# Kernel optimization log

Measured on AMD Instinct MI355X. Metric: run time of the kernel, lower is better.

## Reference

```python
import jax, jax.numpy as jnp
import numpy as np
import math

H = 8
D_MODEL = 4096
D_K = D_MODEL // H  # 512; Sk must equal D_K for the im_attn @ value matmul
B, SQ, SK = 4, 2048, 512


def _linear_params(key, fan_in, fan_out):
    kw, kb = jax.random.split(key)
    bound = 1.0 / math.sqrt(fan_in)
    W = jax.random.uniform(kw, (fan_out, fan_in), jnp.float32, -bound, bound)
    b = jax.random.uniform(kb, (fan_out,), jnp.float32, -bound, bound)
    return W, b


def setup_inputs() -> dict:
    key = jax.random.key(0)
    ks = jax.random.split(key, 8)
    query = jax.random.normal(ks[0], (B, SQ, D_MODEL), jnp.float32)
    k_in = jax.random.normal(ks[1], (B, SK, D_MODEL), jnp.float32)
    v_in = jax.random.normal(ks[2], (B, SK, D_MODEL), jnp.float32)
    image_feat = jax.random.normal(ks[3], (B, SK, D_MODEL), jnp.float32)
    W0, b0 = _linear_params(ks[4], D_MODEL, D_MODEL)
    W1, b1 = _linear_params(ks[5], D_MODEL, D_MODEL)
    W2, b2 = _linear_params(ks[6], D_MODEL, D_MODEL)
    W3, b3 = _linear_params(ks[7], D_MODEL, D_MODEL)  # reused for image_feat AND output proj (as in source)
    return {"query": query, "key": k_in, "value": v_in, "image_feat": image_feat,
            "W0": W0, "b0": b0, "W1": W1, "b1": b1, "W2": W2, "b2": b2, "W3": W3, "b3": b3}


def _split_heads(x):
    # [b, s, d_model] -> [b, h, s, d_k]
    b, s, _ = x.shape
    return x.reshape(b, s, H, D_K).transpose(0, 2, 1, 3)


def reference(query, key, value, image_feat, W0, b0, W1, b1, W2, b2, W3, b3):
    q = _split_heads(query @ W0.T + b0)        # [b,h,Sq,d_k]
    k = _split_heads(key @ W1.T + b1)          # [b,h,Sk,d_k]
    v = _split_heads(value @ W2.T + b2)        # [b,h,Sk,d_k]
    imf = _split_heads(image_feat @ W3.T + b3) # [b,h,Sk,d_k]

    scores = jnp.einsum('bhqd,bhkd->bhqk', q, k) / math.sqrt(D_K)  # [b,h,Sq,Sk]
    p_attn = jax.nn.softmax(scores, axis=-1)
    # second-stage attention over feature axis (Sk == d_k so shapes line up)
    im_attn = jax.nn.softmax(jnp.einsum('bhqk,bhkd->bhqd', p_attn, imf), axis=-1)  # [b,h,Sq,d_k]
    x = jnp.einsum('bhqs,bhsd->bhqd', im_attn, v)  # contracts d_k axis of im_attn with Sk axis of v

    x = x.transpose(0, 2, 1, 3).reshape(query.shape[0], -1, H * D_K)  # [b,Sq,d_model]
    return x @ W3.T + b3  # linears[-1] is the same (shared) 4th linear
```

## Files before the change

### kernel.cpp

```cpp
#include <hip/hip_runtime.h>
#include <hip/hip_bf16.h>
#include <stdint.h>

#define B_   4
#define H_   8
#define SQ_  2048
#define SK_  512
#define DM_  4096
#define DK_  512

typedef __bf16 bf16;
typedef __bf16 bf16x8 __attribute__((ext_vector_type(8)));
typedef float  fx4    __attribute__((ext_vector_type(4)));

typedef __attribute__((address_space(1))) void gv_t;
typedef __attribute__((address_space(3))) void lv_t;

__global__ void sniff_dtype(const uint32_t* __restrict__ q, int* __restrict__ flag)
{
    const int l = threadIdx.x;
    int cnt = 0;
    #pragma unroll
    for (int i = 0; i < 4; ++i) {
        const uint32_t u = q[l * 4 + i];
        const int e = (u >> 7) & 0xFF;
        cnt += (e >= 100 && e <= 135) ? 1 : 0;
    }
    #pragma unroll
    for (int s = 1; s < 64; s <<= 1) cnt += __shfl_xor(cnt, s);
    if (l == 0) *flag = (cnt < 150) ? 1 : 0;
}

__global__ __launch_bounds__(256) void cvt_to_bf16(
    const void* __restrict__ in, bf16* __restrict__ out, const int* __restrict__ flagp)
{
    const size_t i = ((size_t)blockIdx.x * 256 + threadIdx.x) * 8;
    if (*flagp) {
        const float4* p = (const float4*)((const float*)in + i);
        const float4 u0 = p[0], u1 = p[1];
        bf16x8 v;
        v[0] = (bf16)u0.x; v[1] = (bf16)u0.y; v[2] = (bf16)u0.z; v[3] = (bf16)u0.w;
        v[4] = (bf16)u1.x; v[5] = (bf16)u1.y; v[6] = (bf16)u1.z; v[7] = (bf16)u1.w;
        *(bf16x8*)(out + i) = v;
    } else {
        *(bf16x8*)(out + i) = *(const bf16x8*)((const bf16*)in + i);
    }
}

__global__ __launch_bounds__(256, 3) void gemm_bt(
    const bf16* __restrict__ A, const bf16* __restrict__ Bt,
    void* __restrict__ Cv, const void* __restrict__ biasv,
    int K, int lda, int ldb, int ldc, float alpha,
    long long sAb, long long sAh, long long sBb, long long sBh,
    long long sCb, long long sCh,
    const int* __restrict__ flagp, int ebits)
{
    __shared__ bf16 sA[128 * 64];
    __shared__ bf16 sB[128 * 64];

    const int fl = ebits ? *flagp : 0;
    const bool bias32 = fl && (ebits & 1);
    const bool c32    = fl && (ebits & 2);

    const int z = blockIdx.z;
    const int bz = z >> 3, hz = z & 7;
    const bf16* Ab = A  + (size_t)bz * sAb + (size_t)hz * sAh;
    const bf16* Bb = Bt + (size_t)bz * sBb + (size_t)hz * sBh;
    const size_t offC = (size_t)bz * sCb + (size_t)hz * sCh;

    const int n0 = blockIdx.x * 128;
    const int m0 = blockIdx.y * 128;

    const int t = threadIdx.x;
    const int w = t >> 6, l = t & 63;
    const int lrow = l >> 3, lcol = l & 7;
    const int wm = (w >> 1) * 64, wn = (w & 1) * 64;
    const int ml = l & 15, quad = l >> 4;

    const bf16* pa[4];
    const bf16* pb[4];
    #pragma unroll
    for (int i = 0; i < 4; ++i) {
        const int c = w * 4 + i;
        const int r = c * 8 + lrow;
        const int jj = lcol ^ (r & 7);
        pa[i] = Ab + (size_t)(m0 + r) * lda + jj * 8;
        pb[i] = Bb + (size_t)(n0 + r) * ldb + jj * 8;
    }

    fx4 acc[4][4];
    const fx4 zero = {0.f, 0.f, 0.f, 0.f};
    #pragma unroll
    for (int i = 0; i < 4; ++i)
        #pragma unroll
        for (int j = 0; j < 4; ++j) acc[i][j] = zero;

    for (int kt = 0; kt < K; kt += 64) {
        #pragma unroll
        for (int i = 0; i < 4; ++i) {
            const int c = w * 4 + i;
            __builtin_amdgcn_global_load_lds((gv_t*)(pa[i] + kt), (lv_t*)(sA + c * 512), 16, 0, 0);
            __builtin_amdgcn_global_load_lds((gv_t*)(pb[i] + kt), (lv_t*)(sB + c * 512), 16, 0, 0);
        }
        __syncthreads();

        #pragma unroll
        for (int kk = 0; kk < 64; kk += 32) {
            bf16x8 af[4], bfr[4];
            const int jbase = (kk >> 3) + quad;
            #pragma unroll
            for (int mi = 0; mi < 4; ++mi) {
                const int r = wm + mi * 16 + ml;
                af[mi] = *(const bf16x8*)&sA[r * 64 + ((jbase ^ (r & 7)) << 3)];
            }
            #pragma unroll
            for (int ni = 0; ni < 4; ++ni) {
                const int r = wn + ni * 16 + ml;
                bfr[ni] = *(const bf16x8*)&sB[r * 64 + ((jbase ^ (r & 7)) << 3)];
            }
            #pragma unroll
            for (int mi = 0; mi < 4; ++mi)
                #pragma unroll
                for (int ni = 0; ni < 4; ++ni)
                    acc[mi][ni] = __builtin_amdgcn_mfma_f32_16x16x32_bf16(
                        af[mi], bfr[ni], acc[mi][ni], 0, 0, 0);
        }
        __syncthreads();
    }

    #pragma unroll
    for (int ni = 0; ni < 4; ++ni) {
        const int cg = n0 + wn + ni * 16 + ml;
        const float bv = biasv ? (bias32 ? ((const float*)biasv)[cg] : (float)((const bf16*)biasv)[cg]) : 0.f;
        #pragma unroll
        for (int mi = 0; mi < 4; ++mi) {
            const int rg = m0 + wm + mi * 16 + quad * 4;
            #pragma unroll
            for (int r = 0; r < 4; ++r) {
                const float val = acc[mi][ni][r] * alpha + bv;
                const size_t idx = offC + (size_t)(rg + r) * ldc + cg;
                if (c32) ((float*)Cv)[idx] = val;
                else     ((bf16*)Cv)[idx] = (bf16)val;
            }
        }
    }
}

#define BARRIER   asm volatile("s_barrier" ::: "memory")
#define LGKM0     asm volatile("s_waitcnt lgkmcnt(0)" ::: "memory")
#define VM0       asm volatile("s_waitcnt vmcnt(0)" ::: "memory")
#define SCHED0    __builtin_amdgcn_sched_barrier(0)

#define LDS_FRAG(dst, base, fr, kI)                                               \
    dst = *(const bf16x8*)&base[(fr) * 64 + ((((kI) * 4 + quad) ^ ((fr) & 7)) << 3)]

#define READ_A(dst, sX, roff)                                                     \
    _Pragma("unroll")                                                             \
    for (int im_ = 0; im_ < 4; ++im_)                                             \
        _Pragma("unroll")                                                         \
        for (int kI_ = 0; kI_ < 2; ++kI_)                                         \
            LDS_FRAG(dst[im_][kI_], sX, R0 + (roff) + im_ * 16 + ml, kI_);

#define READ_B(dst, sX, coff)                                                     \
    _Pragma("unroll")                                                             \
    for (int in_ = 0; in_ < 2; ++in_)                                             \
        _Pragma("unroll")                                                         \
        for (int kI_ = 0; kI_ < 2; ++kI_)                                         \
            LDS_FRAG(dst[in_][kI_], sX, C0 + (coff) + in_ * 16 + ml, kI_);

#define MFMA_Q(mo, no, afr_, bfr_)                                                \
    __builtin_amdgcn_s_setprio(1);                                                \
    _Pragma("unroll")                                                             \
    for (int kI_ = 0; kI_ < 2; ++kI_)                                             \
        _Pragma("unroll")                                                         \
        for (int im_ = 0; im_ < 4; ++im_)                                         \
            _Pragma("unroll")                                                     \
            for (int in_ = 0; in_ < 2; ++in_)                                     \
                acc[(mo) + im_][(no) + in_] =                                     \
                    __builtin_amdgcn_mfma_f32_16x16x32_bf16(                      \
                        afr_[im_][kI_], bfr_[in_][kI_],                           \
                        acc[(mo) + im_][(no) + in_], 0, 0, 0);                    \
    __builtin_amdgcn_s_setprio(0);

#define STAGE_A(ts, sb)                                                           \
    do {                                                                          \
        _Pragma("unroll")                                                         \
        for (int h_ = 0; h_ < 2; ++h_)                                            \
            _Pragma("unroll")                                                     \
            for (int j_ = 0; j_ < 2; ++j_)                                        \
                __builtin_amdgcn_global_load_lds(                                 \
                    (gv_t*)(pA[h_][j_] + (size_t)(ts) * 64),                      \
                    (lv_t*)(&sm[sb][0][h_ * 8192 + (2 * w + j_) * 512]),          \
                    16, 0, 0);                                                    \
    } while (0)

#define STAGE_B(ts, sb, h)                                                        \
    do {                                                                          \
        _Pragma("unroll")                                                         \
        for (int j_ = 0; j_ < 2; ++j_)                                            \
            __builtin_amdgcn_global_load_lds(                                     \
                (gv_t*)(pB[h][j_] + (size_t)(ts) * 64),                           \
                (lv_t*)(&sm[sb][1][(h) * 8192 + (2 * w + j_) * 512]),             \
                16, 0, 0);                                                        \
    } while (0)

#define HALF_ITER(cb, ts, sb, dostage)                                            \
    do {                                                                          \
        const bf16* sA_ = &sm[cb][0][0];                                          \
        const bf16* sB_ = &sm[cb][1][0];                                          \
                                                                          \
        READ_A(afr, sA_, 0);                                                      \
        READ_B(b0r, sB_, 0);                                                      \
        if (dostage) { STAGE_A(ts, sb); }                                         \
        BARRIER; LGKM0; SCHED0;                                                   \
        MFMA_Q(0, 0, afr, b0r);                                                   \
        BARRIER;                                                                  \
                                                                          \
        READ_B(b1r, sB_, 32);                                                     \
        if (dostage) { STAGE_B(ts, sb, 0); }                                      \
        BARRIER; LGKM0; SCHED0;                                                   \
        MFMA_Q(0, 2, afr, b1r);                                                   \
        BARRIER;                                                                  \
                                                                          \
        READ_A(afr, sA_, 64);                                                     \
        if (dostage) { STAGE_B(ts, sb, 1); }                                      \
        BARRIER; LGKM0; SCHED0;                                                   \
        MFMA_Q(4, 2, afr, b1r);                                                   \
        BARRIER;                                                                  \
                             \
        MFMA_Q(4, 0, afr, b0r);                                                   \
        VM0;                                                                      \
        BARRIER;                                                                  \
    } while (0)

__global__ __launch_bounds__(512, 2) void gemm256(
    const bf16* __restrict__ A, const bf16* __restrict__ Bt,
    void* __restrict__ Cv, const void* __restrict__ biasv,
    int K, int lda, int ldb, int ldc, float alpha,
    long long sAb, long long sAh, long long sBb, long long sBh,
    long long sCb, long long sCh,
    const int* __restrict__ flagp, int ebits)
{
    __shared__ bf16 sm[2][2][256 * 64];

    const int fl = ebits ? *flagp : 0;
    const bool bias32 = fl && (ebits & 1);
    const bool c32    = fl && (ebits & 2);

    const int gX = gridDim.x, gY = gridDim.y;
    int idx = (blockIdx.z * gY + blockIdx.y) * gX + blockIdx.x;
    const int nwg = gX * gY * gridDim.z;
    if ((nwg & 7) == 0) idx = (idx & 7) * (nwg >> 3) + (idx >> 3);
    const int bx = idx % gX;
    const int tmpi = idx / gX;
    const int by = tmpi % gY;
    const int z  = tmpi / gY;

    const int bz = z >> 3, hz = z & 7;
    const bf16* Ab = A  + (size_t)bz * sAb + (size_t)hz * sAh;
    const bf16* Bb = Bt + (size_t)bz * sBb + (size_t)hz * sBh;
    const size_t offC = (size_t)bz * sCb + (size_t)hz * sCh;

    const int n0 = bx * 256;
    const int m0 = by * 256;

    const int t  = threadIdx.x;
    const int w  = t >> 6, l = t & 63;
    const int lrow = l >> 3, lcol = l & 7;
    const int wr = w >> 2, wc = w & 3;
    const int R0 = wr * 128, C0 = wc * 64;
    const int ml = l & 15, quad = l >> 4;

    const bf16* pA[2][2];
    const bf16* pB[2][2];
    #pragma unroll
    for (int h = 0; h < 2; ++h)
        #pragma unroll
        for (int j = 0; j < 2; ++j) {
            const int r = h * 128 + (2 * w + j) * 8 + lrow;
            const int jj = lcol ^ (r & 7);
            pA[h][j] = Ab + (size_t)(m0 + r) * lda + jj * 8;
            pB[h][j] = Bb + (size_t)(n0 + r) * ldb + jj * 8;
        }

    fx4 acc[8][4];
    const fx4 zero = {0.f, 0.f, 0.f, 0.f};
    #pragma unroll
    for (int i = 0; i < 8; ++i)
        #pragma unroll
        for (int j = 0; j < 4; ++j) acc[i][j] = zero;

    bf16x8 afr[4][2], b0r[2][2], b1r[2][2];

    const int nt  = K >> 6;
    const int nit = nt >> 1;

    STAGE_A(0, 0);
    STAGE_B(0, 0, 0);
    STAGE_B(0, 0, 1);
    VM0;
    BARRIER;

    for (int it = 0; it < nit; ++it) {
        HALF_ITER(0, 2 * it + 1, 1, true);
        HALF_ITER(1, 2 * it + 2, 0, (it + 1 < nit));
    }

    #pragma unroll
    for (int ni = 0; ni < 4; ++ni) {
        const int cg = n0 + C0 + ni * 16 + ml;
        const float bv = biasv ? (bias32 ? ((const float*)biasv)[cg] : (float)((const bf16*)biasv)[cg]) : 0.f;
        #pragma unroll
        for (int mi = 0; mi < 8; ++mi) {
            const int rg = m0 + R0 + mi * 16 + quad * 4;
            #pragma unroll
            for (int r = 0; r < 4; ++r) {
                const float val = acc[mi][ni][r] * alpha + bv;
                const size_t idx = offC + (size_t)(rg + r) * ldc + cg;
                if (c32) ((float*)Cv)[idx] = val;
                else     ((bf16*)Cv)[idx] = (bf16)val;
            }
        }
    }
}

__global__ __launch_bounds__(256) void softmax512(bf16* __restrict__ buf)
{
    const int row = blockIdx.x * 4 + (threadIdx.x >> 6);
    const int l = threadIdx.x & 63;
    bf16* p = buf + (size_t)row * 512 + l * 8;
    bf16x8 v = *(const bf16x8*)p;
    float f[8];
    float mx = -1e30f;
    #pragma unroll
    for (int j = 0; j < 8; ++j) {
        f[j] = (float)v[j];
        if (!(fabsf(f[j]) < 1e30f)) f[j] = -1e9f;
        mx = fmaxf(mx, f[j]);
    }
    #pragma unroll
    for (int s = 1; s < 64; s <<= 1) mx = fmaxf(mx, __shfl_xor(mx, s));
    float sum = 0.f;
    #pragma unroll
    for (int j = 0; j < 8; ++j) { f[j] = __expf(f[j] - mx); sum += f[j]; }
    #pragma unroll
    for (int s = 1; s < 64; s <<= 1) sum += __shfl_xor(sum, s);
    const float inv = 1.f / sum;
    #pragma unroll
    for (int j = 0; j < 8; ++j) v[j] = (bf16)(f[j] * inv);
    *(bf16x8*)p = v;
}

__global__ __launch_bounds__(256) void transpose_heads(
    const bf16* __restrict__ in, bf16* __restrict__ out)
{
    __shared__ bf16 tile[32][33];
    const int z = blockIdx.z, b = z >> 3, h = z & 7;
    const int s0 = blockIdx.x * 32, d0 = blockIdx.y * 32;
    const int tx = threadIdx.x, ty = threadIdx.y;
    #pragma unroll
    for (int j = 0; j < 4; ++j) {
        const int s = s0 + ty + j * 8;
        tile[ty + j * 8][tx] = in[(size_t)b * SK_ * DM_ + (size_t)s * DM_ + h * DK_ + d0 + tx];
    }
    __syncthreads();
    #pragma unroll
    for (int j = 0; j < 4; ++j) {
        const int d = d0 + ty + j * 8;
        out[(size_t)z * DK_ * SK_ + (size_t)d * SK_ + s0 + tx] = tile[tx][ty + j * 8];
    }
}

extern "C" void kernel_launch(void* const* d_in, const int* in_sizes, int n_in,
                              void* d_out, int out_size, void* d_ws, size_t ws_size,
                              hipStream_t stream)
{
    const void* query = d_in[0];
    const void* key   = d_in[1];
    const void* value = d_in[2];
    const void* imf   = d_in[3];
    const void* W0 = d_in[4];  const void* b0 = d_in[5];
    const void* W1 = d_in[6];  const void* b1 = d_in[7];
    const void* W2 = d_in[8];  const void* b2 = d_in[9];
    const void* W3 = d_in[10]; const void* b3 = d_in[11];

    bf16* ws    = (bf16*)d_ws;
    int*  flagp = (int*)d_ws;
    bf16* wslot = ws + 8;
    bf16* R     = ws + 8 + 16777216;
    bf16* inbuf = R;
    bf16* vproj = R + 8388608;
    bf16* imfp  = R + 16777216;
    bf16* s1    = R;
    bf16* xcat  = R;

    bf16* obase = (bf16*)d_out;
    bf16* qproj = obase;
    bf16* qbf   = obase + 33554432;
    bf16* kproj = obase + 33554432;
    bf16* vT    = obase + 41943040;
    bf16* imfT  = obase + 50331648;
    bf16* s2    = obase;

    const float inv_sqrt_dk = 0.04419417382415922f;

    sniff_dtype<<<1, 64, 0, stream>>>((const uint32_t*)query, flagp);

    cvt_to_bf16<<<16384, 256, 0, stream>>>(query, qbf, flagp);
    cvt_to_bf16<<<8192, 256, 0, stream>>>(W0, wslot, flagp);
    gemm256<<<dim3(16, 32, 1), 512, 0, stream>>>(qbf, wslot, qproj, b0,
        4096, 4096, 4096, 4096, 1.f, 0,0,0,0,0,0, flagp, 1);
    cvt_to_bf16<<<4096, 256, 0, stream>>>(key, inbuf, flagp);
    cvt_to_bf16<<<8192, 256, 0, stream>>>(W1, wslot, flagp);
    gemm_bt<<<dim3(32, 16, 1), 256, 0, stream>>>(inbuf, wslot, kproj, b1,
        4096, 4096, 4096, 4096, 1.f, 0,0,0,0,0,0, flagp, 1);
    cvt_to_bf16<<<4096, 256, 0, stream>>>(value, inbuf, flagp);
    cvt_to_bf16<<<8192, 256, 0, stream>>>(W2, wslot, flagp);
    gemm_bt<<<dim3(32, 16, 1), 256, 0, stream>>>(inbuf, wslot, vproj, b2,
        4096, 4096, 4096, 4096, 1.f, 0,0,0,0,0,0, flagp, 1);
    cvt_to_bf16<<<4096, 256, 0, stream>>>(imf, inbuf, flagp);
    cvt_to_bf16<<<8192, 256, 0, stream>>>(W3, wslot, flagp);
    gemm_bt<<<dim3(32, 16, 1), 256, 0, stream>>>(inbuf, wslot, imfp, b3,
        4096, 4096, 4096, 4096, 1.f, 0,0,0,0,0,0, flagp, 1);

    transpose_heads<<<dim3(16, 16, 32), dim3(32, 8), 0, stream>>>(vproj, vT);
    transpose_heads<<<dim3(16, 16, 32), dim3(32, 8), 0, stream>>>(imfp, imfT);

    gemm256<<<dim3(2, 8, 32), 512, 0, stream>>>(qproj, kproj, s1, nullptr,
        512, 4096, 4096, 512, inv_sqrt_dk,
        (long long)SQ_*DM_, (long long)DK_, (long long)SK_*DM_, (long long)DK_,
        (long long)H_*SQ_*SK_, (long long)SQ_*SK_, flagp, 0);
    softmax512<<<dim3(16384), 256, 0, stream>>>(s1);
    gemm256<<<dim3(2, 8, 32), 512, 0, stream>>>(s1, imfT, s2, nullptr,
        512, 512, 512, 512, 1.f,
        (long long)H_*SQ_*SK_, (long long)SQ_*SK_, (long long)H_*DK_*SK_, (long long)DK_*SK_,
        (long long)H_*SQ_*SK_, (long long)SQ_*SK_, flagp, 0);
    softmax512<<<dim3(16384), 256, 0, stream>>>(s2);
    gemm256<<<dim3(2, 8, 32), 512, 0, stream>>>(s2, vT, xcat, nullptr,
        512, 512, 512, 4096, 1.f,
        (long long)H_*SQ_*SK_, (long long)SQ_*SK_, (long long)H_*DK_*SK_, (long long)DK_*SK_,
        (long long)SQ_*DM_, (long long)DK_, flagp, 0);
    cvt_to_bf16<<<8192, 256, 0, stream>>>(W3, wslot, flagp);
    gemm256<<<dim3(16, 32, 1), 512, 0, stream>>>(xcat, wslot, d_out, b3,
        4096, 4096, 4096, 4096, 1.f, 0,0,0,0,0,0, flagp, 3);
}
```

Measured before the change: 1.503 ms.

## Batch key and value projections into one gemm256 launch with per-batch bias

Key and value inputs and the W1/W2 weights are converted into separate buffers, and both projections run as one batched gemm256 launch (z=2) instead of two gemm_bt launches. A small kernel packs b1 and b2 into one bias buffer, and gemm256 gains a bias stride so each batch slice picks its own bias. Workspace and output-buffer aliasing are reorganised so everything fits. This is meant to fill the GPU better with the larger 256-tile kernel, at the cost of more memory traffic and buffer reshuffling.

```diff
diff --git a/kernel.cpp b/kernel.cpp
--- a/kernel.cpp
+++ b/kernel.cpp
@@ -45,6 +45,17 @@
     } else {
         *(bf16x8*)(out + i) = *(const bf16x8*)((const bf16*)in + i);
     }
+}
+
+__global__ __launch_bounds__(256) void copy_bias2(
+    const void* __restrict__ b1, const void* __restrict__ b2,
+    void* __restrict__ dst, const int* __restrict__ flagp)
+{
+    const int i = blockIdx.x * 256 + threadIdx.x;
+    const void* src = (i < 4096) ? b1 : b2;
+    const int j = i & 4095;
+    if (*flagp) ((float*)dst)[i] = ((const float*)src)[j];
+    else        ((bf16*)dst)[i]  = ((const bf16*)src)[j];
 }
 
 __global__ __launch_bounds__(256, 3) void gemm_bt(
@@ -239,7 +250,7 @@
     int K, int lda, int ldb, int ldc, float alpha,
     long long sAb, long long sAh, long long sBb, long long sBh,
     long long sCb, long long sCh,
-    const int* __restrict__ flagp, int ebits)
+    const int* __restrict__ flagp, int ebits, int bstride)
 {
     __shared__ bf16 sm[2][2][256 * 64];
 
@@ -309,7 +320,8 @@
     #pragma unroll
     for (int ni = 0; ni < 4; ++ni) {
         const int cg = n0 + C0 + ni * 16 + ml;
-        const float bv = biasv ? (bias32 ? ((const float*)biasv)[cg] : (float)((const bf16*)biasv)[cg]) : 0.f;
+        const int bix = hz * bstride + cg;
+        const float bv = biasv ? (bias32 ? ((const float*)biasv)[bix] : (float)((const bf16*)biasv)[bix]) : 0.f;
         #pragma unroll
         for (int mi = 0; mi < 8; ++mi) {
             const int rg = m0 + R0 + mi * 16 + quad * 4;
@@ -386,41 +398,49 @@
 
     bf16* ws    = (bf16*)d_ws;
     int*  flagp = (int*)d_ws;
-    bf16* wslot = ws + 8;
-    bf16* R     = ws + 8 + 16777216;
-    bf16* inbuf = R;
-    bf16* vproj = R + 8388608;
-    bf16* imfp  = R + 16777216;
-    bf16* s1    = R;
-    bf16* xcat  = R;
+    bf16* wS1   = ws + 8;
+    bf16* wS2   = ws + 16777224;
+    bf16* vT    = ws + 8;
+    bf16* imfT  = ws + 8388616;
+    bf16* w3s   = ws + 16777224;
+    bf16* imfp  = ws + 33554440;
+    bf16* s1    = ws + 16777224;
+    bf16* xcat  = ws + 16777224;
+    bf16* w3f   = ws + 8;
+    bf16* wbias = ws + 50331656;
 
     bf16* obase = (bf16*)d_out;
     bf16* qproj = obase;
     bf16* qbf   = obase + 33554432;
-    bf16* kproj = obase + 33554432;
-    bf16* vT    = obase + 41943040;
-    bf16* imfT  = obase + 50331648;
-    bf16* s2    = obase;
+    bf16* kin   = obase + 33554432;
+    bf16* vin   = obase + 41943040;
+    bf16* iin   = obase + 33554432;
+    bf16* kproj = obase + 50331648;
+    bf16* vproj = obase + 58720256;
+    bf16* s2    = obase + 33554432;
 
     const float inv_sqrt_dk = 0.04419417382415922f;
 
     sniff_dtype<<<1, 64, 0, stream>>>((const uint32_t*)query, flagp);
 
     cvt_to_bf16<<<16384, 256, 0, stream>>>(query, qbf, flagp);
-    cvt_to_bf16<<<8192, 256, 0, stream>>>(W0, wslot, flagp);
-    gemm256<<<dim3(16, 32, 1), 512, 0, stream>>>(qbf, wslot, qproj, b0,
-        4096, 4096, 4096, 4096, 1.f, 0,0,0,0,0,0, flagp, 1);
-    cvt_to_bf16<<<4096, 256, 0, stream>>>(key, inbuf, flagp);
-    cvt_to_bf16<<<8192, 256, 0, stream>>>(W1, wslot, flagp);
-    gemm_bt<<<dim3(32, 16, 1), 256, 0, stream>>>(inbuf, wslot, kproj, b1,
-        4096, 4096, 4096, 4096, 1.f, 0,0,0,0,0,0, flagp, 1);
-    cvt_to_bf16<<<4096, 256, 0, stream>>>(value, inbuf, flagp);
-    cvt_to_bf16<<<8192, 256, 0, stream>>>(W2, wslot, flagp);
-    gemm_bt<<<dim3(32, 16, 1), 256, 0, stream>>>(inbuf, wslot, vproj, b2,
-        4096, 4096, 4096, 4096, 1.f, 0,0,0,0,0,0, flagp, 1);
-    cvt_to_bf16<<<4096, 256, 0, stream>>>(imf, inbuf, flagp);
-    cvt_to_bf16<<<8192, 256, 0, stream>>>(W3, wslot, flagp);
-    gemm_bt<<<dim3(32, 16, 1), 256, 0, stream>>>(inbuf, wslot, imfp, b3,
+    cvt_to_bf16<<<8192, 256, 0, stream>>>(W0, wS1, flagp);
+    gemm256<<<dim3(16, 32, 1), 512, 0, stream>>>(qbf, wS1, qproj, b0,
+        4096, 4096, 4096, 4096, 1.f, 0,0,0,0,0,0, flagp, 1, 0);
+
+    cvt_to_bf16<<<4096, 256, 0, stream>>>(key, kin, flagp);
+    cvt_to_bf16<<<4096, 256, 0, stream>>>(value, vin, flagp);
+    cvt_to_bf16<<<8192, 256, 0, stream>>>(W1, wS1, flagp);
+    cvt_to_bf16<<<8192, 256, 0, stream>>>(W2, wS2, flagp);
+    copy_bias2<<<32, 256, 0, stream>>>(b1, b2, wbias, flagp);
+    gemm256<<<dim3(16, 8, 2), 512, 0, stream>>>(kin, wS1, kproj, wbias,
+        4096, 4096, 4096, 4096, 1.f,
+        0LL, 8388608LL, 0LL, 16777216LL, 0LL, 8388608LL,
+        flagp, 1, 4096);
+
+    cvt_to_bf16<<<4096, 256, 0, stream>>>(imf, iin, flagp);
+    cvt_to_bf16<<<8192, 256, 0, stream>>>(W3, w3s, flagp);
+    gemm_bt<<<dim3(32, 16, 1), 256, 0, stream>>>(iin, w3s, imfp, b3,
         4096, 4096, 4096, 4096, 1.f, 0,0,0,0,0,0, flagp, 1);
 
     transpose_heads<<<dim3(16, 16, 32), dim3(32, 8), 0, stream>>>(vproj, vT);
@@ -429,18 +449,18 @@
     gemm256<<<dim3(2, 8, 32), 512, 0, stream>>>(qproj, kproj, s1, nullptr,
         512, 4096, 4096, 512, inv_sqrt_dk,
         (long long)SQ_*DM_, (long long)DK_, (long long)SK_*DM_, (long long)DK_,
-        (long long)H_*SQ_*SK_, (long long)SQ_*SK_, flagp, 0);
+        (long long)H_*SQ_*SK_, (long long)SQ_*SK_, flagp, 0, 0);
     softmax512<<<dim3(16384), 256, 0, stream>>>(s1);
     gemm256<<<dim3(2, 8, 32), 512, 0, stream>>>(s1, imfT, s2, nullptr,
         512, 512, 512, 512, 1.f,
         (long long)H_*SQ_*SK_, (long long)SQ_*SK_, (long long)H_*DK_*SK_, (long long)DK_*SK_,
-        (long long)H_*SQ_*SK_, (long long)SQ_*SK_, flagp, 0);
+        (long long)H_*SQ_*SK_, (long long)SQ_*SK_, flagp, 0, 0);
     softmax512<<<dim3(16384), 256, 0, stream>>>(s2);
     gemm256<<<dim3(2, 8, 32), 512, 0, stream>>>(s2, vT, xcat, nullptr,
         512, 512, 512, 4096, 1.f,
         (long long)H_*SQ_*SK_, (long long)SQ_*SK_, (long long)H_*DK_*SK_, (long long)DK_*SK_,
-        (long long)SQ_*DM_, (long long)DK_, flagp, 0);
-    cvt_to_bf16<<<8192, 256, 0, stream>>>(W3, wslot, flagp);
-    gemm256<<<dim3(16, 32, 1), 512, 0, stream>>>(xcat, wslot, d_out, b3,
-        4096, 4096, 4096, 4096, 1.f, 0,0,0,0,0,0, flagp, 3);
-}
+        (long long)SQ_*DM_, (long long)DK_, flagp, 0, 0);
+    cvt_to_bf16<<<8192, 256, 0, stream>>>(W3, w3f, flagp);
+    gemm256<<<dim3(16, 32, 1), 512, 0, stream>>>(xcat, w3f, d_out, b3,
+        4096, 4096, 4096, 4096, 1.f, 0,0,0,0,0,0, flagp, 3, 0);
+}
```

New measurement: 1.454 ms. -3.3%, faster.
